# Performance work log

Measured on AMD Instinct MI355X. Metric: run time of the kernel, lower is better.

The kernel has to match this reference:

```python
import jax, jax.numpy as jnp
import numpy as np

B, T, K = 1024, 512, 32


def setup_inputs() -> dict:
    key = jax.random.key(0)
    k1, k2, k3 = jax.random.split(key, 3)
    emissions = jax.random.normal(k1, (B, T, K), dtype=jnp.float32)
    tags = jax.random.randint(k2, (B, T), 0, K)
    mask = jnp.ones((B, T), dtype=bool)
    transitions = jax.random.normal(k3, (K, K), dtype=jnp.float32)
    return {"emissions": emissions, "tags": tags, "mask": mask, "transitions": transitions}


def reference(emissions, tags, mask, transitions):
    # emissions: [B,T,K], tags: [B,T] int, mask: [B,T] bool, transitions: [K,K]
    maskf = mask.astype(emissions.dtype)
    em_t = jnp.swapaxes(emissions, 0, 1)   # [T,B,K]
    mk_t = jnp.swapaxes(mask, 0, 1)        # [T,B]

    # ---- forward algorithm (log partition) ----
    def step(alpha, inp):
        em, m = inp                         # em: [B,K], m: [B]
        # alpha[b,i] + transitions[i,j] -> logsumexp over i, plus emission j
        new = jax.nn.logsumexp(alpha[:, :, None] + transitions[None], axis=1) + em
        alpha = jnp.where(m[:, None], new, alpha)
        return alpha, None

    alpha0 = em_t[0]                        # [B,K] (first step assumed valid)
    alpha, _ = jax.lax.scan(step, alpha0, (em_t[1:], mk_t[1:]))
    log_z = jax.nn.logsumexp(alpha, axis=-1)  # [B]

    # ---- gold path score ----
    em_score = jnp.take_along_axis(emissions, tags[..., None], axis=2)[..., 0]  # [B,T]
    em_score = jnp.sum(em_score * maskf, axis=-1)                               # [B]
    tr = transitions[tags[:, :-1], tags[:, 1:]]                                 # [B,T-1]
    tr_score = jnp.sum(tr * maskf[:, 1:], axis=-1)                              # [B]

    # negative log-likelihood, mean over batch
    loss = jnp.mean(log_z - (em_score + tr_score))
    return loss
```

## Files before the change

### kernel.cpp

```cpp
#include <hip/hip_runtime.h>


#define L2E 1.4426950408889634f
#define LN2 0.6931471805599453f

typedef __attribute__((ext_vector_type(8))) short bf16x8;
typedef __attribute__((ext_vector_type(16))) float f32x16;
typedef __attribute__((ext_vector_type(4))) unsigned u32x4;
typedef __attribute__((ext_vector_type(2))) float f32x2;
typedef __attribute__((ext_vector_type(2))) __bf16 bf16x2;

__device__ __forceinline__ unsigned pk2v(f32x2 t) {
  return __builtin_bit_cast(unsigned, __builtin_convertvector(t, bf16x2));
}
__device__ __forceinline__ unsigned pk2(float lo, float hi) {
  f32x2 t = {lo, hi};
  return pk2v(t);
}

__device__ __forceinline__ bf16x8 mkb(unsigned u0, unsigned u1, unsigned u2, unsigned u3) {
  u32x4 t = {u0, u1, u2, u3};
  return __builtin_bit_cast(bf16x8, t);
}
#define E2(x) __builtin_amdgcn_exp2f((x) * L2E)

__global__ __launch_bounds__(512, 8) void crf_main(
    const float* __restrict__ em, const int* __restrict__ tags,
    const float* __restrict__ trans, float* __restrict__ ws) {
  const int seq  = blockIdx.x;
  const int wid  = threadIdx.x >> 6;
  const int lane = threadIdx.x & 63;
  const int s31  = lane & 31;
  const int h    = lane >> 5;
  const float*  __restrict__ emb  = em + (size_t)seq * (512 * 32);
  const float4* __restrict__ emf4 = (const float4*)emb;

  __shared__ unsigned short sM[8][32][32];
  __shared__ int sCe[8];

  f32x2 EfL2[4], EfH2[4];
#pragma unroll
  for (int j = 0; j < 8; ++j) {
    int kp = (j & 3) + 8 * (j >> 2) + 4 * h;
    EfL2[j >> 1][j & 1] = E2(trans[kp * 32 + s31]);
    EfH2[j >> 1][j & 1] = E2(trans[(16 + kp) * 32 + s31]);
  }

  bf16x8 blo, bhi;
  if (wid == 0) {
    float4 e0 = emf4[h], e1 = emf4[2 + h], e2 = emf4[4 + h], e3 = emf4[6 + h];
    blo = mkb(pk2(E2(e0.x), E2(e0.y)), pk2(E2(e0.z), E2(e0.w)),
              pk2(E2(e1.x), E2(e1.y)), pk2(E2(e1.z), E2(e1.w)));
    bhi = mkb(pk2(E2(e2.x), E2(e2.y)), pk2(E2(e2.z), E2(e2.w)),
              pk2(E2(e3.x), E2(e3.y)), pk2(E2(e3.z), E2(e3.w)));
  } else {
    unsigned v[16];
#pragma unroll
    for (int j = 0; j < 8; ++j) {
      int kp = (j & 3) + 8 * (j >> 2) + 4 * h;
      v[j]     = (kp == s31)        ? 0x3F80u : 0u;
      v[8 + j] = ((16 + kp) == s31) ? 0x3F80u : 0u;
    }
    blo = mkb(v[0] | (v[1] << 16), v[2] | (v[3] << 16),
              v[4] | (v[5] << 16), v[6] | (v[7] << 16));
    bhi = mkb(v[8] | (v[9] << 16), v[10] | (v[11] << 16),
              v[12] | (v[13] << 16), v[14] | (v[15] << 16));
  }

  const int t0     = 1 + 64 * wid;
  const int nsteps = (wid < 7) ? 64 : 63;
  const int rmax = (seq == 1023 && wid == 7) ? 62 : 1 << 20;
  const float* __restrict__ emsp = emb + (size_t)t0 * 32 + s31;

  int   ce = 0, sg = 0;
  float vtrk = 1.0f;
  float cur[4], nxt[4];
#pragma unroll
  for (int i = 0; i < 4; ++i) cur[i] = emsp[32 * i];
#pragma unroll
  for (int i = 0; i < 4; ++i) nxt[i] = emsp[32 * (4 + i)];

  const f32x16 CZ = {};

  auto step = [&](float emt, bool shift, bool track) {
    float pf = __builtin_amdgcn_exp2f(fmaf(emt, L2E, shift ? -(float)sg : 0.0f));
    f32x2 pf2 = {pf, pf};
    unsigned ua[8];
#pragma unroll
    for (int q = 0; q < 4; ++q) {
      ua[q]     = pk2v(pf2 * EfL2[q]);
      ua[4 + q] = pk2v(pf2 * EfH2[q]);
    }
    bf16x8 al = mkb(ua[0], ua[1], ua[2], ua[3]);
    bf16x8 ah = mkb(ua[4], ua[5], ua[6], ua[7]);
    f32x16 D = __builtin_amdgcn_mfma_f32_32x32x16_bf16(al, blo, CZ, 0, 0, 0);
    D = __builtin_amdgcn_mfma_f32_32x32x16_bf16(ah, bhi, D, 0, 0, 0);
    if (track) vtrk = D[0];
    unsigned p[8];
#pragma unroll
    for (int i = 0; i < 4; ++i) {
      f32x2 d0 = {D[4 * i + 0], D[4 * i + 1]};
      f32x2 d1 = {D[4 * i + 2], D[4 * i + 3]};
      p[2 * i]     = pk2v(d0);
      p[2 * i + 1] = pk2v(d1);
    }
    blo = mkb(p[0], p[1], p[2], p[3]);
    bhi = mkb(p[4], p[5], p[6], p[7]);
  };

#pragma unroll 1
  for (int g = 0; g < 15; ++g) {
    step(cur[0], true, false);
    step(cur[1], false, false);
    step(cur[2], false, false);
    step(cur[3], false, true);
#pragma unroll
    for (int i = 0; i < 4; ++i) cur[i] = nxt[i];
    int n0 = 4 * (g + 2);
#pragma unroll
    for (int i = 0; i < 4; ++i) {
      int n = n0 + i;
      n = n > rmax ? rmax : n;
      nxt[i] = emsp[32 * n];
    }
    int xb = __builtin_amdgcn_readlane(__float_as_int(vtrk), 0);
    int s = ((xb >> 23) & 255) - 127;
    s = s < -120 ? -120 : (s > 120 ? 120 : s);
    sg = s; ce += s;
  }
  step(cur[0], true, false);
  step(cur[1], false, false);
  step(cur[2], false, false);
  if (nsteps == 64) step(cur[3], false, false);

  {
    u32x4 xl = __builtin_bit_cast(u32x4, blo);
    u32x4 xh = __builtin_bit_cast(u32x4, bhi);
#pragma unroll
    for (int jj = 0; jj < 4; ++jj) {
      int base = 8 * (jj >> 1) + 4 * h + 2 * (jj & 1);
      sM[wid][base][s31]      = (unsigned short)(xl[jj] & 0xFFFFu);
      sM[wid][base + 1][s31]  = (unsigned short)(xl[jj] >> 16);
      sM[wid][base + 16][s31] = (unsigned short)(xh[jj] & 0xFFFFu);
      sM[wid][base + 17][s31] = (unsigned short)(xh[jj] >> 16);
    }
    if (lane == 0) sCe[wid] = ce;
  }
  __syncthreads();

  if (wid == 1) {
    const int* __restrict__ tgb = tags + (size_t)seq * 512;
    float acc = 0.f;
#pragma unroll
    for (int k = 0; k < 8; ++k) {
      int t = k * 64 + lane;
      int tc = tgb[t];
      acc += emb[t * 32 + tc];
      if (t >= 1) acc += trans[tgb[t - 1] * 32 + tc];
    }
#pragma unroll
    for (int o = 32; o >= 1; o >>= 1) acc += __shfl_xor(acc, o, 64);
    if (lane == 0) ws[1024 + seq] = acc;
    return;
  }
  if (wid != 0) return;

  int ceT = 0;
#pragma unroll
  for (int c = 0; c < 8; ++c) ceT += sCe[c];
  unsigned a0[4], a1[4], b0[4], b1[4];
#pragma unroll
  for (int c = 0; c < 4; ++c) {
    int j0 = 8 * h + 2 * c;
    a0[c] = (unsigned)sM[1][s31][j0]      | ((unsigned)sM[1][s31][j0 + 1] << 16);
    a1[c] = (unsigned)sM[1][s31][16 + j0] | ((unsigned)sM[1][s31][16 + j0 + 1] << 16);
    b0[c] = (unsigned)sM[0][j0][s31]      | ((unsigned)sM[0][j0 + 1][s31] << 16);
    b1[c] = (unsigned)sM[0][16 + j0][s31] | ((unsigned)sM[0][16 + j0 + 1][s31] << 16);
  }
  const f32x16 CZ2 = {};
  f32x16 D = __builtin_amdgcn_mfma_f32_32x32x16_bf16(
      mkb(a0[0], a0[1], a0[2], a0[3]), mkb(b0[0], b0[1], b0[2], b0[3]), CZ2, 0, 0, 0);
  D = __builtin_amdgcn_mfma_f32_32x32x16_bf16(
      mkb(a1[0], a1[1], a1[2], a1[3]), mkb(b1[0], b1[1], b1[2], b1[3]), D, 0, 0, 0);

#pragma unroll 1
  for (int q = 2; q <= 7; ++q) {
    int xb = __builtin_amdgcn_readlane(__float_as_int(D[0]), 0);
    int s = ((xb >> 23) & 255) - 127;
    float sc = __int_as_float((127 - s) << 23);
    ceT += s;
    unsigned p[8];
#pragma unroll
    for (int i = 0; i < 4; ++i) {
      p[2 * i]     = pk2(D[4 * i + 0] * sc, D[4 * i + 1] * sc);
      p[2 * i + 1] = pk2(D[4 * i + 2] * sc, D[4 * i + 3] * sc);
    }
    bf16x8 xb16lo = mkb(p[0], p[1], p[2], p[3]);
    bf16x8 xb16hi = mkb(p[4], p[5], p[6], p[7]);
#pragma unroll
    for (int c = 0; c < 4; ++c) {
      int j0 = 2 * c;
      int kp0 = (j0 & 3) + 8 * (j0 >> 2) + 4 * h;
      a0[c] = (unsigned)sM[q][s31][kp0]      | ((unsigned)sM[q][s31][kp0 + 1] << 16);
      a1[c] = (unsigned)sM[q][s31][16 + kp0] | ((unsigned)sM[q][s31][16 + kp0 + 1] << 16);
    }
    D = __builtin_amdgcn_mfma_f32_32x32x16_bf16(
        mkb(a0[0], a0[1], a0[2], a0[3]), xb16lo, CZ2, 0, 0, 0);
    D = __builtin_amdgcn_mfma_f32_32x32x16_bf16(
        mkb(a1[0], a1[1], a1[2], a1[3]), xb16hi, D, 0, 0, 0);
  }

  float z = 0.f;
#pragma unroll
  for (int r = 0; r < 16; ++r) z += D[r];
  z += __shfl_xor(z, 32, 64);
  if (lane == 0) {
    float logz = LN2 * ((float)ceT + __builtin_amdgcn_logf(z));
    ws[seq] = logz;
  }
}

__global__ void reduce_mean(const float* __restrict__ ws, float* __restrict__ out) {
  __shared__ float sm[4];
  int tid = threadIdx.x;
  float s = 0.f;
#pragma unroll
  for (int i = 0; i < 4; ++i) {
    int idx = tid + 256 * i;
    s += ws[idx] - ws[1024 + idx];
  }
#pragma unroll
  for (int o = 32; o >= 1; o >>= 1) s += __shfl_xor(s, o, 64);
  if ((tid & 63) == 0) sm[tid >> 6] = s;
  __syncthreads();
  if (tid == 0) out[0] = (sm[0] + sm[1] + sm[2] + sm[3]) * (1.0f / 1024.0f);
}

extern "C" void kernel_launch(void* const* d_in, const int* in_sizes, int n_in,
                              void* d_out, int out_size, void* d_ws, size_t ws_size,
                              hipStream_t stream) {
  const float* em    = (const float*)d_in[0];
  const int*   tags  = (const int*)d_in[1];
  const float* trans = (const float*)d_in[3];
  float* ws = (float*)d_ws;

  crf_main<<<1024, 512, 0, stream>>>(em, tags, trans, ws);
  reduce_mean<<<1, 256, 0, stream>>>(ws, (float*)d_out);
}
```

Baseline: 133.6 us.

## Split each wave's time chunk into two interleaved half-chains for MFMA latency hiding

Each wave's 64-step chunk is split in two. The first 32 steps run as an emission-seeded (or identity) chain A and the last 32 as an identity-seeded chain B. The two independent MFMA chains are interleaved in each step so their latencies overlap, halving the serial dependency depth per wave. The halves are combined with one extra 32x32 product per wave before the cross-wave reduction. In exchange the kernel does more MFMA and exp work, adds a lane shuffle per step, and needs an extra syncthreads and extra bf16 rounding and rescaling when the partial matrices are composed.

```diff
diff --git a/kernel.cpp b/kernel.cpp
--- a/kernel.cpp
+++ b/kernel.cpp
@@ -46,14 +46,8 @@
     EfH2[j >> 1][j & 1] = E2(trans[(16 + kp) * 32 + s31]);
   }
 
-  bf16x8 blo, bhi;
-  if (wid == 0) {
-    float4 e0 = emf4[h], e1 = emf4[2 + h], e2 = emf4[4 + h], e3 = emf4[6 + h];
-    blo = mkb(pk2(E2(e0.x), E2(e0.y)), pk2(E2(e0.z), E2(e0.w)),
-              pk2(E2(e1.x), E2(e1.y)), pk2(E2(e1.z), E2(e1.w)));
-    bhi = mkb(pk2(E2(e2.x), E2(e2.y)), pk2(E2(e2.z), E2(e2.w)),
-              pk2(E2(e3.x), E2(e3.y)), pk2(E2(e3.z), E2(e3.w)));
-  } else {
+  bf16x8 bloA, bhiA, bloB, bhiB;
+  {
     unsigned v[16];
 #pragma unroll
     for (int j = 0; j < 8; ++j) {
@@ -61,19 +55,29 @@
       v[j]     = (kp == s31)        ? 0x3F80u : 0u;
       v[8 + j] = ((16 + kp) == s31) ? 0x3F80u : 0u;
     }
-    blo = mkb(v[0] | (v[1] << 16), v[2] | (v[3] << 16),
-              v[4] | (v[5] << 16), v[6] | (v[7] << 16));
-    bhi = mkb(v[8] | (v[9] << 16), v[10] | (v[11] << 16),
-              v[12] | (v[13] << 16), v[14] | (v[15] << 16));
-  }
-
-  const int t0     = 1 + 64 * wid;
-  const int nsteps = (wid < 7) ? 64 : 63;
-  const int rmax = (seq == 1023 && wid == 7) ? 62 : 1 << 20;
-  const float* __restrict__ emsp = emb + (size_t)t0 * 32 + s31;
-
-  int   ce = 0, sg = 0;
-  float vtrk = 1.0f;
+    bf16x8 ilo = mkb(v[0] | (v[1] << 16), v[2] | (v[3] << 16),
+                     v[4] | (v[5] << 16), v[6] | (v[7] << 16));
+    bf16x8 ihi = mkb(v[8] | (v[9] << 16), v[10] | (v[11] << 16),
+                     v[12] | (v[13] << 16), v[14] | (v[15] << 16));
+    bloB = ilo; bhiB = ihi;
+    if (wid == 0) {
+      float4 e0 = emf4[h], e1 = emf4[2 + h], e2 = emf4[4 + h], e3 = emf4[6 + h];
+      bloA = mkb(pk2(E2(e0.x), E2(e0.y)), pk2(E2(e0.z), E2(e0.w)),
+                 pk2(E2(e1.x), E2(e1.y)), pk2(E2(e1.z), E2(e1.w)));
+      bhiA = mkb(pk2(E2(e2.x), E2(e2.y)), pk2(E2(e2.z), E2(e2.w)),
+                 pk2(E2(e3.x), E2(e3.y)), pk2(E2(e3.z), E2(e3.w)));
+    } else {
+      bloA = ilo; bhiA = ihi;
+    }
+  }
+
+  const int t0A = 1 + 64 * wid;
+  const float* __restrict__ emsp = emb + (size_t)(t0A + 32 * h) * 32 + s31;
+  const int rmaxv = (seq == 1023 && wid == 7 && h == 1) ? 30 : 0x0FFFFFFF;
+
+  int   ceA = 0, ceB = 0;
+  float sgv = 0.0f;
+  float vtA = 1.0f, vtB = 1.0f;
   float cur[4], nxt[4];
 #pragma unroll
   for (int i = 0; i < 4; ++i) cur[i] = emsp[32 * i];
@@ -82,8 +86,7 @@
 
   const f32x16 CZ = {};
 
-  auto step = [&](float emt, bool shift, bool track) {
-    float pf = __builtin_amdgcn_exp2f(fmaf(emt, L2E, shift ? -(float)sg : 0.0f));
+  auto stepc = [&](float pf, bf16x8& lo, bf16x8& hi, bool track, float& vt) {
     f32x2 pf2 = {pf, pf};
     unsigned ua[8];
 #pragma unroll
@@ -91,11 +94,11 @@
       ua[q]     = pk2v(pf2 * EfL2[q]);
       ua[4 + q] = pk2v(pf2 * EfH2[q]);
     }
-    bf16x8 al = mkb(ua[0], ua[1], ua[2], ua[3]);
-    bf16x8 ah = mkb(ua[4], ua[5], ua[6], ua[7]);
-    f32x16 D = __builtin_amdgcn_mfma_f32_32x32x16_bf16(al, blo, CZ, 0, 0, 0);
-    D = __builtin_amdgcn_mfma_f32_32x32x16_bf16(ah, bhi, D, 0, 0, 0);
-    if (track) vtrk = D[0];
+    f32x16 D = __builtin_amdgcn_mfma_f32_32x32x16_bf16(
+        mkb(ua[0], ua[1], ua[2], ua[3]), lo, CZ, 0, 0, 0);
+    D = __builtin_amdgcn_mfma_f32_32x32x16_bf16(
+        mkb(ua[4], ua[5], ua[6], ua[7]), hi, D, 0, 0, 0);
+    if (track) vt = D[0];
     unsigned p[8];
 #pragma unroll
     for (int i = 0; i < 4; ++i) {
@@ -104,38 +107,61 @@
       p[2 * i]     = pk2v(d0);
       p[2 * i + 1] = pk2v(d1);
     }
-    blo = mkb(p[0], p[1], p[2], p[3]);
-    bhi = mkb(p[4], p[5], p[6], p[7]);
+    lo = mkb(p[0], p[1], p[2], p[3]);
+    hi = mkb(p[4], p[5], p[6], p[7]);
   };
 
+  auto pair = [&](float ec, bool shift, bool track) {
+    float x   = shift ? fmaf(ec, L2E, sgv) : ec * L2E;
+    float pfo = __builtin_amdgcn_exp2f(x);
+    float pfs = __shfl_xor(pfo, 32, 64);
+    float pfA = h ? pfs : pfo;
+    float pfB = h ? pfo : pfs;
+    stepc(pfA, bloA, bhiA, track, vtA);
+    stepc(pfB, bloB, bhiB, track, vtB);
+  };
+
 #pragma unroll 1
-  for (int g = 0; g < 15; ++g) {
-    step(cur[0], true, false);
-    step(cur[1], false, false);
-    step(cur[2], false, false);
-    step(cur[3], false, true);
+  for (int g = 0; g < 7; ++g) {
+    pair(cur[0], true, false);
+    pair(cur[1], false, false);
+    pair(cur[2], false, false);
+    pair(cur[3], false, true);
 #pragma unroll
     for (int i = 0; i < 4; ++i) cur[i] = nxt[i];
     int n0 = 4 * (g + 2);
 #pragma unroll
     for (int i = 0; i < 4; ++i) {
       int n = n0 + i;
-      n = n > rmax ? rmax : n;
+      n = n > rmaxv ? rmaxv : n;
       nxt[i] = emsp[32 * n];
     }
-    int xb = __builtin_amdgcn_readlane(__float_as_int(vtrk), 0);
-    int s = ((xb >> 23) & 255) - 127;
-    s = s < -120 ? -120 : (s > 120 ? 120 : s);
-    sg = s; ce += s;
-  }
-  step(cur[0], true, false);
-  step(cur[1], false, false);
-  step(cur[2], false, false);
-  if (nsteps == 64) step(cur[3], false, false);
+    int xa = __builtin_amdgcn_readlane(__float_as_int(vtA), 0);
+    int sa = ((xa >> 23) & 255) - 127;
+    sa = sa < -120 ? -120 : (sa > 120 ? 120 : sa);
+    ceA += sa;
+    int xb = __builtin_amdgcn_readlane(__float_as_int(vtB), 0);
+    int sb = ((xb >> 23) & 255) - 127;
+    sb = sb < -120 ? -120 : (sb > 120 ? 120 : sb);
+    ceB += sb;
+    sgv = h ? -(float)sb : -(float)sa;
+  }
+  pair(cur[0], true, false);
+  pair(cur[1], false, false);
+  pair(cur[2], false, false);
+  if (wid < 7) {
+    pair(cur[3], false, false);
+  } else {
+    float x   = cur[3] * L2E;
+    float pfo = __builtin_amdgcn_exp2f(x);
+    float pfs = __shfl_xor(pfo, 32, 64);
+    float pfA = h ? pfs : pfo;
+    stepc(pfA, bloA, bhiA, false, vtA);
+  }
 
   {
-    u32x4 xl = __builtin_bit_cast(u32x4, blo);
-    u32x4 xh = __builtin_bit_cast(u32x4, bhi);
+    u32x4 xl = __builtin_bit_cast(u32x4, bloB);
+    u32x4 xh = __builtin_bit_cast(u32x4, bhiB);
 #pragma unroll
     for (int jj = 0; jj < 4; ++jj) {
       int base = 8 * (jj >> 1) + 4 * h + 2 * (jj & 1);
@@ -144,8 +170,38 @@
       sM[wid][base + 16][s31] = (unsigned short)(xh[jj] & 0xFFFFu);
       sM[wid][base + 17][s31] = (unsigned short)(xh[jj] >> 16);
     }
-    if (lane == 0) sCe[wid] = ce;
-  }
+  }
+  __syncthreads();
+
+  f32x16 D;
+  {
+    unsigned a0[4], a1[4];
+#pragma unroll
+    for (int c = 0; c < 4; ++c) {
+      int j0 = 2 * c;
+      int kp0 = (j0 & 3) + 8 * (j0 >> 2) + 4 * h;
+      a0[c] = (unsigned)sM[wid][s31][kp0]      | ((unsigned)sM[wid][s31][kp0 + 1] << 16);
+      a1[c] = (unsigned)sM[wid][s31][16 + kp0] | ((unsigned)sM[wid][s31][16 + kp0 + 1] << 16);
+    }
+    D = __builtin_amdgcn_mfma_f32_32x32x16_bf16(
+        mkb(a0[0], a0[1], a0[2], a0[3]), bloA, CZ, 0, 0, 0);
+    D = __builtin_amdgcn_mfma_f32_32x32x16_bf16(
+        mkb(a1[0], a1[1], a1[2], a1[3]), bhiA, D, 0, 0, 0);
+  }
+  int ceP = ceA + ceB;
+  if (wid != 0) {
+    int xb = __builtin_amdgcn_readlane(__float_as_int(D[0]), 0);
+    int s = ((xb >> 23) & 255) - 127;
+    s = s < -120 ? -120 : (s > 120 ? 120 : s);
+    float sc = __int_as_float((127 - s) << 23);
+    ceP += s;
+#pragma unroll
+    for (int r = 0; r < 16; ++r) {
+      int row = (r & 3) + 8 * (r >> 2) + 4 * h;
+      sM[wid][row][s31] = (unsigned short)(pk2(D[r] * sc, 0.0f) & 0xFFFFu);
+    }
+  }
+  if (lane == 0) sCe[wid] = ceP;
   __syncthreads();
 
   if (wid == 1) {
@@ -168,23 +224,9 @@
   int ceT = 0;
 #pragma unroll
   for (int c = 0; c < 8; ++c) ceT += sCe[c];
-  unsigned a0[4], a1[4], b0[4], b1[4];
-#pragma unroll
-  for (int c = 0; c < 4; ++c) {
-    int j0 = 8 * h + 2 * c;
-    a0[c] = (unsigned)sM[1][s31][j0]      | ((unsigned)sM[1][s31][j0 + 1] << 16);
-    a1[c] = (unsigned)sM[1][s31][16 + j0] | ((unsigned)sM[1][s31][16 + j0 + 1] << 16);
-    b0[c] = (unsigned)sM[0][j0][s31]      | ((unsigned)sM[0][j0 + 1][s31] << 16);
-    b1[c] = (unsigned)sM[0][16 + j0][s31] | ((unsigned)sM[0][16 + j0 + 1][s31] << 16);
-  }
-  const f32x16 CZ2 = {};
-  f32x16 D = __builtin_amdgcn_mfma_f32_32x32x16_bf16(
-      mkb(a0[0], a0[1], a0[2], a0[3]), mkb(b0[0], b0[1], b0[2], b0[3]), CZ2, 0, 0, 0);
-  D = __builtin_amdgcn_mfma_f32_32x32x16_bf16(
-      mkb(a1[0], a1[1], a1[2], a1[3]), mkb(b1[0], b1[1], b1[2], b1[3]), D, 0, 0, 0);
 
 #pragma unroll 1
-  for (int q = 2; q <= 7; ++q) {
+  for (int q = 1; q <= 7; ++q) {
     int xb = __builtin_amdgcn_readlane(__float_as_int(D[0]), 0);
     int s = ((xb >> 23) & 255) - 127;
     float sc = __int_as_float((127 - s) << 23);
@@ -197,6 +239,7 @@
     }
     bf16x8 xb16lo = mkb(p[0], p[1], p[2], p[3]);
     bf16x8 xb16hi = mkb(p[4], p[5], p[6], p[7]);
+    unsigned a0[4], a1[4];
 #pragma unroll
     for (int c = 0; c < 4; ++c) {
       int j0 = 2 * c;
@@ -205,7 +248,7 @@
       a1[c] = (unsigned)sM[q][s31][16 + kp0] | ((unsigned)sM[q][s31][16 + kp0 + 1] << 16);
     }
     D = __builtin_amdgcn_mfma_f32_32x32x16_bf16(
-        mkb(a0[0], a0[1], a0[2], a0[3]), xb16lo, CZ2, 0, 0, 0);
+        mkb(a0[0], a0[1], a0[2], a0[3]), xb16lo, CZ, 0, 0, 0);
     D = __builtin_amdgcn_mfma_f32_32x32x16_bf16(
         mkb(a1[0], a1[1], a1[2], a1[3]), xb16hi, D, 0, 0, 0);
   }
```

After: 155.1 us. 16.1% more time.
